# Kernel optimization log

Hardware: AMD Instinct MI355X
Metric: run time of the kernel (lower is better)

The kernel has to match this reference:

```python
import jax, jax.numpy as jnp
import numpy as np

EPS = 1e-8  # torch.cosine_similarity clamps norms at eps=1e-8


def setup_inputs() -> dict:
    key = jax.random.key(0)
    k1, k2, k3 = jax.random.split(key, 3)
    B, C, D = 256, 128, 1024
    return {
        "doc_emb": jax.random.normal(k1, (B, D), dtype=jnp.float32),
        "summary_emb": jax.random.normal(k2, (B, D), dtype=jnp.float32),
        "candidate_emb": jax.random.normal(k3, (B, C, D), dtype=jnp.float32),
    }


def _clamped_norm(x):
    return jnp.maximum(jnp.linalg.norm(x, axis=-1), EPS)


def reference(doc_emb, summary_emb, candidate_emb):
    # doc_emb: [B, D], summary_emb: [B, D], candidate_emb: [B, C, D]
    B, C, D = candidate_emb.shape
    dn = _clamped_norm(doc_emb)          # [B]
    sn = _clamped_norm(summary_emb)      # [B]
    cn = _clamped_norm(candidate_emb)    # [B, C]

    # outer_score[b,c] = cos(candidate[b,c], doc[b])
    outer_score = jnp.einsum("bcd,bd->bc", candidate_emb, doc_emb) / (cn * dn[:, None])

    # inner_score: replaces the O(B*C^2) python loop with one batched Gram matmul.
    chat = candidate_emb / cn[:, :, None]           # unit candidates [B, C, D]
    gram = jnp.einsum("bcd,bkd->bck", chat, chat)    # [B, C, C] cosine sims
    diag = jnp.einsum("bcc->bc", gram)               # self-similarity (==1)
    inner_score = (gram.sum(axis=-1) - diag) / (C - 1)  # mean over _cn != cn

    # summary_score[b] = cos(summary[b], doc[b])
    summary_score = jnp.einsum("bd,bd->b", summary_emb, doc_emb) / (sn * dn)

    # summary_avg_score[b] = mean_c cos(summary[b], candidate[b,c])
    sc = jnp.einsum("bd,bcd->bc", summary_emb, candidate_emb) / (sn[:, None] * cn)
    summary_avg_score = sc.mean(axis=-1)

    return (outer_score, inner_score, summary_score, summary_avg_score)
```

## Files before the change

kernel.cpp:

```cpp
#include <hip/hip_runtime.h>
#include <math.h>


#define EPS 1e-8f
constexpr int B = 256;
constexpr int C = 128;
constexpr int D = 1024;
constexpr int NW = 16;
constexpr int CPW = C / NW;

__device__ __forceinline__ float dot4(const float4 a, const float4 b) {
    return a.x * b.x + a.y * b.y + a.z * b.z + a.w * b.w;
}

__global__ __launch_bounds__(1024) void rerank_all(
    const float* __restrict__ doc, const float* __restrict__ summ,
    const float* __restrict__ cand, float* __restrict__ out_outer,
    float* __restrict__ out_inner, float* __restrict__ out_sumscore,
    float* __restrict__ out_sumavg) {
    const int b = blockIdx.x;
    const int t = threadIdx.x;
    const int wave = t >> 6;
    const int lane = t & 63;

    __shared__ float4 dmd[D / 4];
    __shared__ float4 dms[D / 4];
    __shared__ float s_part[NW][D];
    __shared__ float s_full[D];
    __shared__ float ic_lds[C];
    __shared__ float sa_lds[NW];

    if (t < 256) dmd[t] = ((const float4*)(doc + (size_t)b * D))[t];
    else if (t < 512) dms[t - 256] = ((const float4*)(summ + (size_t)b * D))[t - 256];
#pragma unroll
    for (int q = 0; q < 4; ++q)
        ((float4*)s_part[wave])[lane + 64 * q] = make_float4(0.f, 0.f, 0.f, 0.f);
    __syncthreads();

    float dd = 0.0f, ss = 0.0f, sd = 0.0f;
#pragma unroll
    for (int q = 0; q < 4; ++q) {
        const float4 d = dmd[lane + 64 * q];
        const float4 m = dms[lane + 64 * q];
        dd += dot4(d, d);
        ss += dot4(m, m);
        sd += dot4(m, d);
    }
#pragma unroll
    for (int lv = 1; lv <= 32; lv <<= 1) {
        dd += __shfl_xor(dd, lv, 64);
        ss += __shfl_xor(ss, lv, 64);
        sd += __shfl_xor(sd, lv, 64);
    }
    const float di = 1.0f / fmaxf(sqrtf(dd), EPS);
    const float si = 1.0f / fmaxf(sqrtf(ss), EPS);
    if (t == 0) out_sumscore[b] = sd * di * si;

    const float4* cb = (const float4*)(cand + (size_t)b * C * D);
    float* sw = s_part[wave];

    float sa_acc = 0.0f;
#pragma unroll
    for (int p = 0; p < CPW / 2; ++p) {
        const int c0 = wave * CPW + 2 * p;
        const float4* cp0 = cb + (size_t)c0 * (D / 4);
        const float4* cp1 = cp0 + (D / 4);
        float4 cv0[4], cv1[4];
#pragma unroll
        for (int q = 0; q < 4; ++q) {
            cv0[q] = cp0[lane + 64 * q];
            cv1[q] = cp1[lane + 64 * q];
        }
        float cc0 = 0.f, cd0 = 0.f, cs0 = 0.f;
        float cc1 = 0.f, cd1 = 0.f, cs1 = 0.f;
#pragma unroll
        for (int q = 0; q < 4; ++q) {
            const float4 d = dmd[lane + 64 * q];
            const float4 m = dms[lane + 64 * q];
            cc0 += dot4(cv0[q], cv0[q]);
            cd0 += dot4(cv0[q], d);
            cs0 += dot4(cv0[q], m);
            cc1 += dot4(cv1[q], cv1[q]);
            cd1 += dot4(cv1[q], d);
            cs1 += dot4(cv1[q], m);
        }
#pragma unroll
        for (int lv = 1; lv <= 32; lv <<= 1) {
            cc0 += __shfl_xor(cc0, lv, 64);
            cd0 += __shfl_xor(cd0, lv, 64);
            cs0 += __shfl_xor(cs0, lv, 64);
            cc1 += __shfl_xor(cc1, lv, 64);
            cd1 += __shfl_xor(cd1, lv, 64);
            cs1 += __shfl_xor(cs1, lv, 64);
        }
        const float icv0 = 1.0f / fmaxf(sqrtf(cc0), EPS);
        const float icv1 = 1.0f / fmaxf(sqrtf(cc1), EPS);
        sa_acc += cs0 * icv0 + cs1 * icv1;
        if (lane == 0) {
            out_outer[b * C + c0] = cd0 * icv0 * di;
            out_outer[b * C + c0 + 1] = cd1 * icv1 * di;
            ic_lds[c0] = icv0;
            ic_lds[c0 + 1] = icv1;
        }
#pragma unroll
        for (int q = 0; q < 4; ++q) {
            float4 cur = ((float4*)sw)[lane + 64 * q];
            cur.x += cv0[q].x * icv0 + cv1[q].x * icv1;
            cur.y += cv0[q].y * icv0 + cv1[q].y * icv1;
            cur.z += cv0[q].z * icv0 + cv1[q].z * icv1;
            cur.w += cv0[q].w * icv0 + cv1[q].w * icv1;
            ((float4*)sw)[lane + 64 * q] = cur;
        }
    }
    if (lane == 0) sa_lds[wave] = sa_acc;
    __syncthreads();

    float colsum = 0.0f;
#pragma unroll
    for (int w = 0; w < NW; ++w) colsum += s_part[w][t];
    s_full[t] = colsum;
    if (t == 0) {
        float S = 0.0f;
#pragma unroll
        for (int w = 0; w < NW; ++w) S += sa_lds[w];
        out_sumavg[b] = S * si * (1.0f / C);
    }
    __syncthreads();

#pragma unroll
    for (int p = 0; p < CPW / 2; ++p) {
        const int c0 = wave * CPW + 2 * p;
        const float4* cp0 = cb + (size_t)c0 * (D / 4);
        const float4* cp1 = cp0 + (D / 4);
        float td0 = 0.f, td1 = 0.f;
#pragma unroll
        for (int q = 0; q < 4; ++q) {
            const float4 sv = ((const float4*)s_full)[lane + 64 * q];
            td0 += dot4(cp0[lane + 64 * q], sv);
            td1 += dot4(cp1[lane + 64 * q], sv);
        }
#pragma unroll
        for (int lv = 1; lv <= 32; lv <<= 1) {
            td0 += __shfl_xor(td0, lv, 64);
            td1 += __shfl_xor(td1, lv, 64);
        }
        if (lane == 0) {
            out_inner[b * C + c0] =
                (td0 * ic_lds[c0] - 1.0f) * (1.0f / (C - 1));
            out_inner[b * C + c0 + 1] =
                (td1 * ic_lds[c0 + 1] - 1.0f) * (1.0f / (C - 1));
        }
    }
}

extern "C" void kernel_launch(void* const* d_in, const int* in_sizes, int n_in,
                              void* d_out, int out_size, void* d_ws,
                              size_t ws_size, hipStream_t stream) {
    const float* doc = (const float*)d_in[0];
    const float* summ = (const float*)d_in[1];
    const float* cand = (const float*)d_in[2];

    float* out = (float*)d_out;
    float* out_outer = out;
    float* out_inner = out + B * C;
    float* out_sumscore = out + 2 * B * C;
    float* out_sumavg = out + 2 * B * C + B;

    rerank_all<<<B, 1024, 0, stream>>>(doc, summ, cand, out_outer, out_inner,
                                       out_sumscore, out_sumavg);
}
```

Before: 216.9 us.

## Split per-batch kernel into two kernels with quarter-batch blocks and atomic reduction

Replaces the single 1024-thread-per-batch kernel with two kernels launched over 4x more 256-thread blocks, each handling a quarter of the candidates. The first kernel computes norms, outer and summary scores, and accumulates the normalized candidate sum into a global workspace with atomicAdd. The second re-reads the candidates to compute inner scores against the global sum. This aims for better occupancy and load balance across CUs, at the cost of extra launches, memsets, global atomics, and a second pass over the candidate tensor that may now miss cache.

Measured after the change: 222.1 us. +2.4%, slower.

```diff
diff --git a/kernel.cpp b/kernel.cpp
--- a/kernel.cpp
+++ b/kernel.cpp
@@ -6,19 +6,23 @@
 constexpr int B = 256;
 constexpr int C = 128;
 constexpr int D = 1024;
-constexpr int NW = 16;
-constexpr int CPW = C / NW;
+constexpr int QB = 4;
+constexpr int CPB = C / QB;
+constexpr int NW = 4;
+constexpr int CPW = CPB / NW;
 
 __device__ __forceinline__ float dot4(const float4 a, const float4 b) {
     return a.x * b.x + a.y * b.y + a.z * b.z + a.w * b.w;
 }
 
-__global__ __launch_bounds__(1024) void rerank_all(
+__global__ __launch_bounds__(256) void k1_stream(
     const float* __restrict__ doc, const float* __restrict__ summ,
     const float* __restrict__ cand, float* __restrict__ out_outer,
-    float* __restrict__ out_inner, float* __restrict__ out_sumscore,
-    float* __restrict__ out_sumavg) {
-    const int b = blockIdx.x;
+    float* __restrict__ out_sumscore, float* __restrict__ out_sumavg,
+    float* __restrict__ ic_ws, float* __restrict__ s_ws) {
+    const int blk = blockIdx.x;
+    const int b = blk >> 2;
+    const int q4 = blk & 3;
     const int t = threadIdx.x;
     const int wave = t >> 6;
     const int lane = t & 63;
@@ -26,22 +30,20 @@
     __shared__ float4 dmd[D / 4];
     __shared__ float4 dms[D / 4];
     __shared__ float s_part[NW][D];
-    __shared__ float s_full[D];
-    __shared__ float ic_lds[C];
-    __shared__ float sa_lds[NW];
+    __shared__ float sa_l[NW];
 
-    if (t < 256) dmd[t] = ((const float4*)(doc + (size_t)b * D))[t];
-    else if (t < 512) dms[t - 256] = ((const float4*)(summ + (size_t)b * D))[t - 256];
+    dmd[t] = ((const float4*)(doc + (size_t)b * D))[t];
+    dms[t] = ((const float4*)(summ + (size_t)b * D))[t];
 #pragma unroll
-    for (int q = 0; q < 4; ++q)
-        ((float4*)s_part[wave])[lane + 64 * q] = make_float4(0.f, 0.f, 0.f, 0.f);
+    for (int j = 0; j < 4; ++j)
+        ((float4*)s_part[wave])[lane + 64 * j] = make_float4(0.f, 0.f, 0.f, 0.f);
     __syncthreads();
 
     float dd = 0.0f, ss = 0.0f, sd = 0.0f;
 #pragma unroll
-    for (int q = 0; q < 4; ++q) {
-        const float4 d = dmd[lane + 64 * q];
-        const float4 m = dms[lane + 64 * q];
+    for (int j = 0; j < 4; ++j) {
+        const float4 d = dmd[lane + 64 * j];
+        const float4 m = dms[lane + 64 * j];
         dd += dot4(d, d);
         ss += dot4(m, m);
         sd += dot4(m, d);
@@ -54,35 +56,35 @@
     }
     const float di = 1.0f / fmaxf(sqrtf(dd), EPS);
     const float si = 1.0f / fmaxf(sqrtf(ss), EPS);
-    if (t == 0) out_sumscore[b] = sd * di * si;
+    if (q4 == 0 && t == 0) out_sumscore[b] = sd * di * si;
 
     const float4* cb = (const float4*)(cand + (size_t)b * C * D);
     float* sw = s_part[wave];
+    float sa_acc = 0.0f;
 
-    float sa_acc = 0.0f;
 #pragma unroll
     for (int p = 0; p < CPW / 2; ++p) {
-        const int c0 = wave * CPW + 2 * p;
+        const int c0 = q4 * CPB + wave * CPW + 2 * p;
         const float4* cp0 = cb + (size_t)c0 * (D / 4);
         const float4* cp1 = cp0 + (D / 4);
         float4 cv0[4], cv1[4];
 #pragma unroll
-        for (int q = 0; q < 4; ++q) {
-            cv0[q] = cp0[lane + 64 * q];
-            cv1[q] = cp1[lane + 64 * q];
+        for (int j = 0; j < 4; ++j) {
+            cv0[j] = cp0[lane + 64 * j];
+            cv1[j] = cp1[lane + 64 * j];
         }
         float cc0 = 0.f, cd0 = 0.f, cs0 = 0.f;
         float cc1 = 0.f, cd1 = 0.f, cs1 = 0.f;
 #pragma unroll
-        for (int q = 0; q < 4; ++q) {
-            const float4 d = dmd[lane + 64 * q];
-            const float4 m = dms[lane + 64 * q];
-            cc0 += dot4(cv0[q], cv0[q]);
-            cd0 += dot4(cv0[q], d);
-            cs0 += dot4(cv0[q], m);
-            cc1 += dot4(cv1[q], cv1[q]);
-            cd1 += dot4(cv1[q], d);
-            cs1 += dot4(cv1[q], m);
+        for (int j = 0; j < 4; ++j) {
+            const float4 d = dmd[lane + 64 * j];
+            const float4 m = dms[lane + 64 * j];
+            cc0 += dot4(cv0[j], cv0[j]);
+            cd0 += dot4(cv0[j], d);
+            cs0 += dot4(cv0[j], m);
+            cc1 += dot4(cv1[j], cv1[j]);
+            cd1 += dot4(cv1[j], d);
+            cs1 += dot4(cv1[j], m);
         }
 #pragma unroll
         for (int lv = 1; lv <= 32; lv <<= 1) {
@@ -99,45 +101,61 @@
         if (lane == 0) {
             out_outer[b * C + c0] = cd0 * icv0 * di;
             out_outer[b * C + c0 + 1] = cd1 * icv1 * di;
-            ic_lds[c0] = icv0;
-            ic_lds[c0 + 1] = icv1;
+            ic_ws[b * C + c0] = icv0;
+            ic_ws[b * C + c0 + 1] = icv1;
         }
 #pragma unroll
-        for (int q = 0; q < 4; ++q) {
-            float4 cur = ((float4*)sw)[lane + 64 * q];
-            cur.x += cv0[q].x * icv0 + cv1[q].x * icv1;
-            cur.y += cv0[q].y * icv0 + cv1[q].y * icv1;
-            cur.z += cv0[q].z * icv0 + cv1[q].z * icv1;
-            cur.w += cv0[q].w * icv0 + cv1[q].w * icv1;
-            ((float4*)sw)[lane + 64 * q] = cur;
+        for (int j = 0; j < 4; ++j) {
+            float4 cur = ((float4*)sw)[lane + 64 * j];
+            cur.x += cv0[j].x * icv0 + cv1[j].x * icv1;
+            cur.y += cv0[j].y * icv0 + cv1[j].y * icv1;
+            cur.z += cv0[j].z * icv0 + cv1[j].z * icv1;
+            cur.w += cv0[j].w * icv0 + cv1[j].w * icv1;
+            ((float4*)sw)[lane + 64 * j] = cur;
         }
     }
-    if (lane == 0) sa_lds[wave] = sa_acc;
+    if (lane == 0) sa_l[wave] = sa_acc;
     __syncthreads();
 
-    float colsum = 0.0f;
+    float* sb = s_ws + (size_t)b * D;
 #pragma unroll
-    for (int w = 0; w < NW; ++w) colsum += s_part[w][t];
-    s_full[t] = colsum;
-    if (t == 0) {
-        float S = 0.0f;
-#pragma unroll
-        for (int w = 0; w < NW; ++w) S += sa_lds[w];
-        out_sumavg[b] = S * si * (1.0f / C);
+    for (int j = 0; j < 4; ++j) {
+        const int col = t + 256 * j;
+        const float v =
+            s_part[0][col] + s_part[1][col] + s_part[2][col] + s_part[3][col];
+        atomicAdd(&sb[col], v);
     }
+    if (t == 0)
+        atomicAdd(&out_sumavg[b],
+                  (sa_l[0] + sa_l[1] + sa_l[2] + sa_l[3]) * si * (1.0f / C));
+}
+
+__global__ __launch_bounds__(256) void k2_inner(
+    const float* __restrict__ cand, const float* __restrict__ s_ws,
+    const float* __restrict__ ic_ws, float* __restrict__ out_inner) {
+    const int blk = blockIdx.x;
+    const int b = blk >> 2;
+    const int q4 = blk & 3;
+    const int t = threadIdx.x;
+    const int wave = t >> 6;
+    const int lane = t & 63;
+
+    __shared__ float4 sl[D / 4];
+    sl[t] = ((const float4*)(s_ws + (size_t)b * D))[t];
     __syncthreads();
 
+    const float4* cb = (const float4*)(cand + (size_t)b * C * D);
 #pragma unroll
     for (int p = 0; p < CPW / 2; ++p) {
-        const int c0 = wave * CPW + 2 * p;
+        const int c0 = q4 * CPB + wave * CPW + 2 * p;
         const float4* cp0 = cb + (size_t)c0 * (D / 4);
         const float4* cp1 = cp0 + (D / 4);
         float td0 = 0.f, td1 = 0.f;
 #pragma unroll
-        for (int q = 0; q < 4; ++q) {
-            const float4 sv = ((const float4*)s_full)[lane + 64 * q];
-            td0 += dot4(cp0[lane + 64 * q], sv);
-            td1 += dot4(cp1[lane + 64 * q], sv);
+        for (int j = 0; j < 4; ++j) {
+            const float4 sv = sl[lane + 64 * j];
+            td0 += dot4(cp0[lane + 64 * j], sv);
+            td1 += dot4(cp1[lane + 64 * j], sv);
         }
 #pragma unroll
         for (int lv = 1; lv <= 32; lv <<= 1) {
@@ -146,9 +164,9 @@
         }
         if (lane == 0) {
             out_inner[b * C + c0] =
-                (td0 * ic_lds[c0] - 1.0f) * (1.0f / (C - 1));
+                (td0 * ic_ws[b * C + c0] - 1.0f) * (1.0f / (C - 1));
             out_inner[b * C + c0 + 1] =
-                (td1 * ic_lds[c0 + 1] - 1.0f) * (1.0f / (C - 1));
+                (td1 * ic_ws[b * C + c0 + 1] - 1.0f) * (1.0f / (C - 1));
         }
     }
 }
@@ -166,6 +184,15 @@
     float* out_sumscore = out + 2 * B * C;
     float* out_sumavg = out + 2 * B * C + B;
 
-    rerank_all<<<B, 1024, 0, stream>>>(doc, summ, cand, out_outer, out_inner,
-                                       out_sumscore, out_sumavg);
+    float* ws = (float*)d_ws;
+    float* s_ws = ws;
+    float* ic_ws = ws + B * D;
+
+    hipMemsetAsync(s_ws, 0, (size_t)B * D * sizeof(float), stream);
+    hipMemsetAsync(out_sumavg, 0, B * sizeof(float), stream);
+
+    k1_stream<<<B * QB, 256, 0, stream>>>(doc, summ, cand, out_outer,
+                                          out_sumscore, out_sumavg, ic_ws,
+                                          s_ws);
+    k2_inner<<<B * QB, 256, 0, stream>>>(cand, s_ws, ic_ws, out_inner);
 }
```
